# Kernel tuning notes

Hardware: AMD Instinct MI355X
Metric: run time of the kernel (lower is better)

## Reference

```python
import jax, jax.numpy as jnp
import numpy as np

VX, VY = 0.16, 0.16
X0, Y0 = 0.0, -39.68
BN_EPS = 1e-5
P, M, C_IN, C_OUT = 40000, 100, 9, 64


def setup_inputs() -> dict:
    key = jax.random.key(0)
    ks = jax.random.split(key, 8)
    return {
        "pillar_x": jax.random.normal(ks[0], (P, M), dtype=jnp.float32),
        "pillar_y": jax.random.normal(ks[1], (P, M), dtype=jnp.float32),
        "pillar_z": jax.random.normal(ks[2], (P, M), dtype=jnp.float32),
        "pillar_i": jax.random.uniform(ks[3], (P, M), dtype=jnp.float32),
        "num_points_per_pillar": jax.random.randint(ks[4], (P,), 0, M, dtype=jnp.int32),
        "coors": jax.random.randint(ks[5], (P, 4), 0, 496, dtype=jnp.int32),
        "W": jax.random.normal(ks[6], (C_IN, C_OUT), dtype=jnp.float32) * 0.1,
        "gamma": jnp.ones((C_OUT,), dtype=jnp.float32),
        "beta": jnp.zeros((C_OUT,), dtype=jnp.float32),
    }


def reference(pillar_x, pillar_y, pillar_z, pillar_i, num_points_per_pillar, coors, W, gamma, beta):
    dtype = pillar_x.dtype
    max_points = pillar_x.shape[1]
    # per-pillar point count, clamped to >=1 (matches torch.clamp(min=1))
    n = jnp.clip(num_points_per_pillar, 1, None).astype(dtype)[:, None]  # (P,1)
    mean_x = jnp.sum(pillar_x, axis=1, keepdims=True) / n
    mean_y = jnp.sum(pillar_y, axis=1, keepdims=True) / n
    mean_z = jnp.sum(pillar_z, axis=1, keepdims=True) / n
    x_off = pillar_x - mean_x
    y_off = pillar_y - mean_y
    z_off = pillar_z - mean_z
    # BEV pillar-center coordinates, broadcast over points
    x_bev = (coors[:, 3].astype(dtype) * VX + VX / 2 + X0)[:, None] * jnp.ones((1, max_points), dtype)
    y_bev = (coors[:, 2].astype(dtype) * VY + VY / 2 + Y0)[:, None] * jnp.ones((1, max_points), dtype)
    # validity mask: point index < num_points (vectorized version of the python loop)
    mask = (jnp.arange(max_points)[None, :] < num_points_per_pillar[:, None]).astype(dtype)
    feats = jnp.stack(
        [pillar_x, pillar_y, pillar_z, pillar_i, x_off, y_off, z_off, x_bev, y_bev],
        axis=-1,
    )  # (P, M, 9)
    feats = feats * mask[:, :, None]
    # PFNLayer: Linear (no bias) -> BatchNorm1d (training-mode batch stats) -> ReLU -> max over points
    x = jnp.einsum("pmc,cd->pmd", feats, W)  # (P, M, 64)
    mu = jnp.mean(x, axis=(0, 1))
    var = jnp.var(x, axis=(0, 1))  # biased variance, as BatchNorm uses
    x = (x - mu) * jax.lax.rsqrt(var + BN_EPS) * gamma + beta
    x = jax.nn.relu(x)
    return jnp.max(x, axis=1)  # (P, 64)
```

## Files before the change

kernel.cpp:

```cpp
#include <hip/hip_runtime.h>

#define P_N 40000
#define M_N 100
#define NBF 2500
#define NPART 80
#define NUSED 74

typedef _Float16 half2_t __attribute__((ext_vector_type(2)));

__device__ __forceinline__ float bcf(int x) { return __int_as_float(x); }
__device__ __forceinline__ int   bci(float x) { return __float_as_int(x); }
__device__ __forceinline__ float rlf(float v, int l) {
  return bcf(__builtin_amdgcn_readlane(bci(v), l));
}
__device__ __forceinline__ int pk16i(float a, float b) {
  return __builtin_bit_cast(int, __builtin_amdgcn_cvt_pkrtz(a, b));
}
__device__ __forceinline__ half2_t h2(int x) { return __builtin_bit_cast(half2_t, x); }
__device__ __forceinline__ float dot2(int a, int b, float acc) {
  return __builtin_amdgcn_fdot2(h2(a), h2(b), acc, false);
}

__device__ __forceinline__ float dpp_sum64(float x) {
  x += bcf(__builtin_amdgcn_update_dpp(0, bci(x), 0x111, 0xf, 0xf, true));
  x += bcf(__builtin_amdgcn_update_dpp(0, bci(x), 0x112, 0xf, 0xf, true));
  x += bcf(__builtin_amdgcn_update_dpp(0, bci(x), 0x114, 0xf, 0xf, true));
  x += bcf(__builtin_amdgcn_update_dpp(0, bci(x), 0x118, 0xf, 0xf, true));
  x += bcf(__builtin_amdgcn_update_dpp(0, bci(x), 0x142, 0xf, 0xf, true));
  x += bcf(__builtin_amdgcn_update_dpp(0, bci(x), 0x143, 0xf, 0xf, true));
  return x;
}

__device__ __forceinline__ float uPT(int xy, int zi, half2_t AB, half2_t CD, float sE) {
  return __builtin_amdgcn_fdot2(h2(xy), AB,
         __builtin_amdgcn_fdot2(h2(zi), CD, sE, false), false);
}


__global__ __launch_bounds__(256) void k_fused(
    const float* __restrict__ px, const float* __restrict__ py,
    const float* __restrict__ pz, const float* __restrict__ pi,
    const int* __restrict__ npp, const int* __restrict__ coors,
    const float* __restrict__ W,
    float* __restrict__ partials, float* __restrict__ umm)
{
  const int lane = threadIdx.x & 63;
  const int wid  = threadIdx.x >> 6;
  const int d    = lane;

  __shared__ int4  stage[4][4][64];
  __shared__ float red[4][NPART];

  int c = 9, c2 = 9;
  if (lane < 45) {
    int k = lane; c = 0;
    while (k >= 9 - c) { k -= 9 - c; ++c; }
    c2 = c + k;
  } else if (lane < 54) {
    c = lane - 45; c2 = 9;
  }
  const int rc1 = (c  < 4) ? c  : (c  < 7) ? c  - 4 : (c  < 9) ? c  - 2 : 4;
  const int rc2 = (c2 < 4) ? c2 : (c2 < 7) ? c2 - 4 : (c2 < 9) ? c2 - 2 : 4;
  const bool bothVec = (rc1 < 4) && (rc2 < 4);
  const bool statln  = lane < 54;

  float w[9];
  #pragma unroll
  for (int q = 0; q < 9; ++q) w[q] = W[q * 64 + d];
  const float sA = w[0] + w[4], sB = w[1] + w[5], sC = w[2] + w[6], sD = w[3];
  const half2_t AB = h2(pk16i(sA, sB));
  const half2_t CD = h2(pk16i(sC, sD));
  const int H1 = 0x3C003C00;

  const bool act = lane < 50;
  const int wgid  = blockIdx.x * 4 + wid;
  const int pbase = __builtin_amdgcn_readfirstlane(wgid * 4);

  const int4 n4 = ((const int4*)npp)[wgid];
  int4 cc[4];
  #pragma unroll
  for (int it = 0; it < 4; ++it) cc[it] = ((const int4*)coors)[pbase + it];

  int u0[4], u1[4], u2[4], u3[4];
  #pragma unroll
  for (int it = 0; it < 4; ++it) {
    const int p_ = pbase + it;
    float2 X = make_float2(0.f, 0.f), Y = X, Z = X, I = X;
    if (act) {
      X = ((const float2*)(px + (size_t)p_ * M_N))[lane];
      Y = ((const float2*)(py + (size_t)p_ * M_N))[lane];
      Z = ((const float2*)(pz + (size_t)p_ * M_N))[lane];
      I = ((const float2*)(pi + (size_t)p_ * M_N))[lane];
    }
    u0[it] = pk16i(X.x, X.y);
    u1[it] = pk16i(Y.x, Y.y);
    u2[it] = pk16i(Z.x, Z.y);
    u3[it] = pk16i(I.x, I.y);
    int4 pm;
    pm.x = pk16i(X.x, Y.x);
    pm.y = pk16i(Z.x, I.x);
    pm.z = pk16i(X.y, Y.y);
    pm.w = pk16i(Z.y, I.y);
    stage[wid][it][lane] = pm;
  }

  float R2a[10] = {};
  float corrAcc = 0.f;

  #pragma unroll
  for (int it = 0; it < 4; ++it) {
    const int p_ = pbase + it;
    const int n  = ((const int*)&n4)[it];
    const float nf = (float)n;

    const unsigned msk = ((2 * lane     < n) ? 0x0000FFFFu : 0u)
                       | ((2 * lane + 1 < n) ? 0xFFFF0000u : 0u);
    const int g0 = u0[it] & msk;
    const int g1 = u1[it] & msk;
    const int g2 = u2[it] & msk;
    const int g3 = u3[it] & msk;

    float fx = dot2(u0[it], H1, 0.f);
    float fy = dot2(u1[it], H1, 0.f);
    float fz = dot2(u2[it], H1, 0.f);
    float vx = dot2(g0, H1, 0.f);
    float vy = dot2(g1, H1, 0.f);
    float vz = dot2(g2, H1, 0.f);
    float vi = dot2(g3, H1, 0.f);
    fx = dpp_sum64(fx); fy = dpp_sum64(fy); fz = dpp_sum64(fz);
    vx = dpp_sum64(vx); vy = dpp_sum64(vy); vz = dpp_sum64(vz); vi = dpp_sum64(vi);

    const int nc = n < 1 ? 1 : n;
    const float inv = __builtin_amdgcn_rcpf((float)nc);
    const float mx = rlf(fx, 63) * inv;
    const float my = rlf(fy, 63) * inv;
    const float mz = rlf(fz, 63) * inv;
    const float svx = rlf(vx, 63);
    const float svy = rlf(vy, 63);
    const float svz = rlf(vz, 63);
    const float svi = rlf(vi, 63);

    const float xb = fmaf((float)cc[it].w, 0.16f, 0.08f);
    const float yb = fmaf((float)cc[it].z, 0.16f, 0.08f - 39.68f);

    R2a[0] = dot2(g0, g0, R2a[0]);
    R2a[1] = dot2(g0, g1, R2a[1]);
    R2a[2] = dot2(g0, g2, R2a[2]);
    R2a[3] = dot2(g0, g3, R2a[3]);
    R2a[4] = dot2(g1, g1, R2a[4]);
    R2a[5] = dot2(g1, g2, R2a[5]);
    R2a[6] = dot2(g1, g3, R2a[6]);
    R2a[7] = dot2(g2, g2, R2a[7]);
    R2a[8] = dot2(g2, g3, R2a[8]);
    R2a[9] = dot2(g3, g3, R2a[9]);

    {
      const float nxb = nf * xb, nyb = nf * yb;
      const float S1 = (rc1 == 0) ? svx : (rc1 == 1) ? svy : (rc1 == 2) ? svz
                     : (rc1 == 3) ? svi : (rc1 == 4) ? nf  : (rc1 == 5) ? nxb : nyb;
      const float S2 = (rc2 == 0) ? svx : (rc2 == 1) ? svy : (rc2 == 2) ? svz
                     : (rc2 == 3) ? svi : (rc2 == 4) ? nf  : (rc2 == 5) ? nxb : nyb;
      float base = 0.f;
      if (!bothVec)
        base = (rc1 > 3) ? ((rc1 == 4) ? S2 : (rc1 == 5) ? xb * S2 : yb * S2)
                         : ((rc2 == 4) ? S1 : (rc2 == 5) ? xb * S1 : yb * S1);
      const float mv1 = (c  == 4) ? mx : (c  == 5) ? my : (c  == 6) ? mz : 0.f;
      const float mv2 = (c2 == 4) ? mx : (c2 == 5) ? my : (c2 == 6) ? mz : 0.f;
      const float term = base - mv1 * S2 - mv2 * S1 + nf * mv1 * mv2;
      if (statln) corrAcc += term;
    }

    const float sE = fmaf(-mx, w[4], fmaf(-my, w[5], fmaf(-mz, w[6],
                     fmaf(xb, w[7], yb * w[8]))));

    const int4* sp = &stage[wid][it][0];
    float um0 = -3.0e38f, um1 = -3.0e38f;
    const int nq = n >> 2;
    for (int l = 0; l < nq; ++l) {
      const int4 qa = sp[2 * l];
      const int4 qb = sp[2 * l + 1];
      const float v0 = uPT(qa.x, qa.y, AB, CD, sE);
      const float v1 = uPT(qa.z, qa.w, AB, CD, sE);
      const float v2 = uPT(qb.x, qb.y, AB, CD, sE);
      const float v3 = uPT(qb.z, qb.w, AB, CD, sE);
      um0 = fmaxf(fmaxf(um0, v0), v1);
      um1 = fmaxf(fmaxf(um1, v2), v3);
    }
    const int m_ = nq * 4;
    if (n - m_ >= 2) {
      const int4 qa = sp[m_ >> 1];
      const float v0 = uPT(qa.x, qa.y, AB, CD, sE);
      const float v1 = uPT(qa.z, qa.w, AB, CD, sE);
      um0 = fmaxf(fmaxf(um0, v0), v1);
    }
    if (n & 1) {
      const int2 qq = ((const int2*)sp)[n - 1];
      um1 = fmaxf(um1, uPT(qq.x, qq.y, AB, CD, sE));
    }
    umm[(size_t)p_ * 64 + d] = fmaxf(um0, um1);
  }

  #pragma unroll
  for (int i = 0; i < 10; ++i) R2a[i] = dpp_sum64(R2a[i]);

  red[wid][lane] = corrAcc;
  if (lane == 63) {
    #pragma unroll
    for (int i = 0; i < 10; ++i) red[wid][64 + i] = R2a[i];
  }
  __syncthreads();
  if (threadIdx.x < NUSED) {
    const int t = threadIdx.x;
    partials[blockIdx.x * NPART + t] = red[0][t] + red[1][t] + red[2][t] + red[3][t];
  }
}


__global__ __launch_bounds__(256) void k_red(
    const float* __restrict__ partials, float* __restrict__ stats)
{
  const int c = blockIdx.x;
  float s = 0.f;
  for (int b = threadIdx.x; b < NBF; b += 256) s += partials[b * NPART + c];
  s = dpp_sum64(s);
  __shared__ float r4[4];
  const int lane = threadIdx.x & 63, wid = threadIdx.x >> 6;
  if (lane == 63) r4[wid] = s;
  __syncthreads();
  if (threadIdx.x == 0) stats[c] = r4[0] + r4[1] + r4[2] + r4[3];
}


__global__ __launch_bounds__(64) void k_stats(
    const float* __restrict__ stats, const float* __restrict__ W,
    const float* __restrict__ gamma, const float* __restrict__ beta,
    float* __restrict__ scale, float* __restrict__ shift)
{
  const int d = threadIdx.x;
  __shared__ float Cs[NUSED];
  Cs[d] = stats[d];
  if (d < NUSED - 64) Cs[64 + d] = stats[64 + d];
  __syncthreads();

  float mom1[9];
  #pragma unroll
  for (int q = 0; q < 9; ++q) mom1[q] = Cs[45 + q];
  float mom2[45];
  {
    int k = 0;
    #pragma unroll
    for (int cA = 0; cA < 9; ++cA) {
      #pragma unroll
      for (int cB = cA; cB < 9; ++cB) {
        float v = Cs[k];
        if (cA <= 6 && cB <= 6) {
          const int a = (cA < 4) ? cA : cA - 4;
          const int b = (cB < 4) ? cB : cB - 4;
          const int lo = a < b ? a : b;
          const int hi = a < b ? b : a;
          const int idx = lo * 4 - lo * (lo - 1) / 2 + (hi - lo);
          v += Cs[64 + idx];
        }
        mom2[k] = v;
        ++k;
      }
    }
  }

  float w[9];
  #pragma unroll
  for (int q = 0; q < 9; ++q) w[q] = W[q * 64 + d];
  const float invN = 1.f / ((float)P_N * (float)M_N);
  float mu = 0.f;
  #pragma unroll
  for (int q = 0; q < 9; ++q) mu += mom1[q] * w[q];
  mu *= invN;
  float e2 = 0.f;
  int k = 0;
  #pragma unroll
  for (int cA = 0; cA < 9; ++cA) {
    #pragma unroll
    for (int cB = cA; cB < 9; ++cB) {
      const float t = w[cA] * w[cB] * mom2[k];
      e2 += (cA == cB) ? t : 2.f * t;
      ++k;
    }
  }
  e2 *= invN;
  float var = e2 - mu * mu;
  var = var < 0.f ? 0.f : var;
  const float sc = gamma[d] * rsqrtf(var + 1e-5f);
  const float sh = fmaf(-mu, sc, beta[d]);
  scale[d] = sc;
  shift[d] = sh;
}


__global__ __launch_bounds__(256) void k_apply(
    const int* __restrict__ npp, const float* __restrict__ scale,
    const float* __restrict__ shift, float* __restrict__ out)
{
  const int gid = blockIdx.x * 256 + threadIdx.x;
  const int p = gid >> 4;
  const int q = gid & 15;

  float4 u4 = ((const float4*)out)[gid];
  const float4 sc4 = ((const float4*)scale)[q];
  const float4 sh4 = ((const float4*)shift)[q];
  const int n = npp[p];
  const bool has_masked = n < M_N;

  float4 r;
  float t;
  t = fmaf(sc4.x, u4.x, sh4.x); if (has_masked) t = fmaxf(t, sh4.x); r.x = fmaxf(t, 0.f);
  t = fmaf(sc4.y, u4.y, sh4.y); if (has_masked) t = fmaxf(t, sh4.y); r.y = fmaxf(t, 0.f);
  t = fmaf(sc4.z, u4.z, sh4.z); if (has_masked) t = fmaxf(t, sh4.z); r.z = fmaxf(t, 0.f);
  t = fmaf(sc4.w, u4.w, sh4.w); if (has_masked) t = fmaxf(t, sh4.w); r.w = fmaxf(t, 0.f);
  ((float4*)out)[gid] = r;
}


extern "C" void kernel_launch(void* const* d_in, const int* in_sizes, int n_in,
                              void* d_out, int out_size, void* d_ws, size_t ws_size,
                              hipStream_t stream) {
  const float* px    = (const float*)d_in[0];
  const float* py    = (const float*)d_in[1];
  const float* pz    = (const float*)d_in[2];
  const float* pi    = (const float*)d_in[3];
  const int*   npp   = (const int*)d_in[4];
  const int*   coors = (const int*)d_in[5];
  const float* W     = (const float*)d_in[6];
  const float* gamma = (const float*)d_in[7];
  const float* beta  = (const float*)d_in[8];
  float* out = (float*)d_out;

  float* wsf      = (float*)d_ws;
  float* partials = wsf;
  float* stats    = wsf + 200000;
  float* scale    = wsf + 200128;
  float* shift    = wsf + 200192;

  k_fused<<<NBF, 256, 0, stream>>>(px, py, pz, pi, npp, coors, W, partials, out);
  k_red<<<NUSED, 256, 0, stream>>>(partials, stats);
  k_stats<<<1, 64, 0, stream>>>(stats, W, gamma, beta, scale, shift);
  k_apply<<<P_N * 64 / 4 / 256, 256, 0, stream>>>(npp, scale, shift, out);
}
```

Baseline: 55.58 us.

## Use packed fp16 FMA/max for per-point projection and shrink blocks to 128 threads

The per-point linear projection and max now use packed half2 FMA and elementwise max: two points are evaluated per instruction with fp16 accumulation, replacing fp32 dot2 accumulation. The stage layout changes to hold per-channel packed pairs. Blocks drop to 2 waves with 2 pillars per wave, which quadruples the grid and the partials buffer. The aim is fewer VALU instructions in the inner loop and more parallelism, at the cost of fp16 rounding in the accumulated projection and more work for the partials reduction.

```diff
diff --git a/kernel.cpp b/kernel.cpp
--- a/kernel.cpp
+++ b/kernel.cpp
@@ -2,7 +2,7 @@
 
 #define P_N 40000
 #define M_N 100
-#define NBF 2500
+#define NBF 10000
 #define NPART 80
 #define NUSED 74
 
@@ -31,13 +31,17 @@
   return x;
 }
 
-__device__ __forceinline__ float uPT(int xy, int zi, half2_t AB, half2_t CD, float sE) {
-  return __builtin_amdgcn_fdot2(h2(xy), AB,
-         __builtin_amdgcn_fdot2(h2(zi), CD, sE, false), false);
-}
-
-
-__global__ __launch_bounds__(256) void k_fused(
+__device__ __forceinline__ half2_t uPK(int4 q, half2_t AA, half2_t BB,
+                                       half2_t CC, half2_t DD, half2_t EE) {
+  half2_t t = h2(q.w) * DD + EE;
+  t = h2(q.z) * CC + t;
+  t = h2(q.y) * BB + t;
+  t = h2(q.x) * AA + t;
+  return t;
+}
+
+
+__global__ __launch_bounds__(128) void k_fused(
     const float* __restrict__ px, const float* __restrict__ py,
     const float* __restrict__ pz, const float* __restrict__ pi,
     const int* __restrict__ npp, const int* __restrict__ coors,
@@ -48,8 +52,8 @@
   const int wid  = threadIdx.x >> 6;
   const int d    = lane;
 
-  __shared__ int4  stage[4][4][64];
-  __shared__ float red[4][NPART];
+  __shared__ int4  stage[2][2][64];
+  __shared__ float red[2][NPART];
 
   int c = 9, c2 = 9;
   if (lane < 45) {
@@ -68,22 +72,24 @@
   #pragma unroll
   for (int q = 0; q < 9; ++q) w[q] = W[q * 64 + d];
   const float sA = w[0] + w[4], sB = w[1] + w[5], sC = w[2] + w[6], sD = w[3];
-  const half2_t AB = h2(pk16i(sA, sB));
-  const half2_t CD = h2(pk16i(sC, sD));
+  const half2_t AA = h2(pk16i(sA, sA));
+  const half2_t BB = h2(pk16i(sB, sB));
+  const half2_t CC = h2(pk16i(sC, sC));
+  const half2_t DD = h2(pk16i(sD, sD));
   const int H1 = 0x3C003C00;
 
   const bool act = lane < 50;
-  const int wgid  = blockIdx.x * 4 + wid;
-  const int pbase = __builtin_amdgcn_readfirstlane(wgid * 4);
-
-  const int4 n4 = ((const int4*)npp)[wgid];
-  int4 cc[4];
-  #pragma unroll
-  for (int it = 0; it < 4; ++it) cc[it] = ((const int4*)coors)[pbase + it];
-
-  int u0[4], u1[4], u2[4], u3[4];
-  #pragma unroll
-  for (int it = 0; it < 4; ++it) {
+  const int wgid  = blockIdx.x * 2 + wid;
+  const int pbase = __builtin_amdgcn_readfirstlane(wgid * 2);
+
+  const int2 n2 = ((const int2*)npp)[wgid];
+  int4 cc[2];
+  cc[0] = ((const int4*)coors)[pbase + 0];
+  cc[1] = ((const int4*)coors)[pbase + 1];
+
+  int u0[2], u1[2], u2[2], u3[2];
+  #pragma unroll
+  for (int it = 0; it < 2; ++it) {
     const int p_ = pbase + it;
     float2 X = make_float2(0.f, 0.f), Y = X, Z = X, I = X;
     if (act) {
@@ -96,21 +102,16 @@
     u1[it] = pk16i(Y.x, Y.y);
     u2[it] = pk16i(Z.x, Z.y);
     u3[it] = pk16i(I.x, I.y);
-    int4 pm;
-    pm.x = pk16i(X.x, Y.x);
-    pm.y = pk16i(Z.x, I.x);
-    pm.z = pk16i(X.y, Y.y);
-    pm.w = pk16i(Z.y, I.y);
-    stage[wid][it][lane] = pm;
+    stage[wid][it][lane] = make_int4(u0[it], u1[it], u2[it], u3[it]);
   }
 
   float R2a[10] = {};
   float corrAcc = 0.f;
 
   #pragma unroll
-  for (int it = 0; it < 4; ++it) {
+  for (int it = 0; it < 2; ++it) {
     const int p_ = pbase + it;
-    const int n  = ((const int*)&n4)[it];
+    const int n  = ((const int*)&n2)[it];
     const float nf = (float)n;
 
     const unsigned msk = ((2 * lane     < n) ? 0x0000FFFFu : 0u)
@@ -172,32 +173,32 @@
 
     const float sE = fmaf(-mx, w[4], fmaf(-my, w[5], fmaf(-mz, w[6],
                      fmaf(xb, w[7], yb * w[8]))));
+    const half2_t EE = h2(pk16i(sE, sE));
 
     const int4* sp = &stage[wid][it][0];
-    float um0 = -3.0e38f, um1 = -3.0e38f;
-    const int nq = n >> 2;
-    for (int l = 0; l < nq; ++l) {
-      const int4 qa = sp[2 * l];
-      const int4 qb = sp[2 * l + 1];
-      const float v0 = uPT(qa.x, qa.y, AB, CD, sE);
-      const float v1 = uPT(qa.z, qa.w, AB, CD, sE);
-      const float v2 = uPT(qb.x, qb.y, AB, CD, sE);
-      const float v3 = uPT(qb.z, qb.w, AB, CD, sE);
-      um0 = fmaxf(fmaxf(um0, v0), v1);
-      um1 = fmaxf(fmaxf(um1, v2), v3);
-    }
-    const int m_ = nq * 4;
-    if (n - m_ >= 2) {
-      const int4 qa = sp[m_ >> 1];
-      const float v0 = uPT(qa.x, qa.y, AB, CD, sE);
-      const float v1 = uPT(qa.z, qa.w, AB, CD, sE);
-      um0 = fmaxf(fmaxf(um0, v0), v1);
-    }
+    half2_t ap0 = h2((int)0xFC00FC00);
+    half2_t ap1 = ap0;
+    const int nh = n >> 1;
+    int l = 0;
+    for (; l + 2 <= nh; l += 2) {
+      const int4 qa = sp[l];
+      const int4 qb = sp[l + 1];
+      ap0 = __builtin_elementwise_max(ap0, uPK(qa, AA, BB, CC, DD, EE));
+      ap1 = __builtin_elementwise_max(ap1, uPK(qb, AA, BB, CC, DD, EE));
+    }
+    if (l < nh)
+      ap0 = __builtin_elementwise_max(ap0, uPK(sp[l], AA, BB, CC, DD, EE));
+    const half2_t am = __builtin_elementwise_max(ap0, ap1);
+    float um = fmaxf((float)am.x, (float)am.y);
     if (n & 1) {
-      const int2 qq = ((const int2*)sp)[n - 1];
-      um1 = fmaxf(um1, uPT(qq.x, qq.y, AB, CD, sE));
-    }
-    umm[(size_t)p_ * 64 + d] = fmaxf(um0, um1);
+      const int4 qt = sp[nh];
+      const float tx = (float)h2(qt.x).x;
+      const float ty = (float)h2(qt.y).x;
+      const float tz = (float)h2(qt.z).x;
+      const float ti = (float)h2(qt.w).x;
+      um = fmaxf(um, fmaf(tx, sA, fmaf(ty, sB, fmaf(tz, sC, fmaf(ti, sD, sE)))));
+    }
+    umm[(size_t)p_ * 64 + d] = um;
   }
 
   #pragma unroll
@@ -211,7 +212,7 @@
   __syncthreads();
   if (threadIdx.x < NUSED) {
     const int t = threadIdx.x;
-    partials[blockIdx.x * NPART + t] = red[0][t] + red[1][t] + red[2][t] + red[3][t];
+    partials[blockIdx.x * NPART + t] = red[0][t] + red[1][t];
   }
 }
 
@@ -336,11 +337,11 @@
 
   float* wsf      = (float*)d_ws;
   float* partials = wsf;
-  float* stats    = wsf + 200000;
-  float* scale    = wsf + 200128;
-  float* shift    = wsf + 200192;
-
-  k_fused<<<NBF, 256, 0, stream>>>(px, py, pz, pi, npp, coors, W, partials, out);
+  float* stats    = wsf + 800000;
+  float* scale    = wsf + 800128;
+  float* shift    = wsf + 800192;
+
+  k_fused<<<NBF, 128, 0, stream>>>(px, py, pz, pi, npp, coors, W, partials, out);
   k_red<<<NUSED, 256, 0, stream>>>(partials, stats);
   k_stats<<<1, 64, 0, stream>>>(stats, W, gamma, beta, scale, shift);
   k_apply<<<P_N * 64 / 4 / 256, 256, 0, stream>>>(npp, scale, shift, out);
```

Result: slower. 64.37 us (+15.8%).
